# Kernel tuning notes

Measured on AMD Instinct MI355X. Metric: run time of the kernel, lower is better.

## Reference

```python
import jax, jax.numpy as jnp
import numpy as np

B, T, D, H = 64, 512, 768, 96


def setup_inputs() -> dict:
    key = jax.random.key(0)
    kx, kq, kk, kv = jax.random.split(key, 4)
    x = jax.random.normal(kx, (B, T, D), dtype=jnp.float32)
    # Linear weights stored as [in, out]; scaled like torch default init
    s = 1.0 / np.sqrt(D)
    Wq = jax.random.normal(kq, (D, H), dtype=jnp.float32) * s
    Wk = jax.random.normal(kk, (D, H), dtype=jnp.float32) * s
    Wv = jax.random.normal(kv, (D, H), dtype=jnp.float32) * s
    return {"x": x, "Wq": Wq, "Wk": Wk, "Wv": Wv}


def reference(x, Wq, Wk, Wv):
    # q,k,v: [B,T,H]
    q = jnp.einsum('btd,dh->bth', x, Wq)
    k = jnp.einsum('btd,dh->bth', x, Wk)
    v = jnp.einsum('btd,dh->bth', x, Wv)
    scale = 1.0 / jnp.sqrt(jnp.array(q.shape[-1], dtype=x.dtype))
    # scores: [B,T,T]
    wei = jnp.einsum('bqh,bkh->bqk', q, k) * scale
    causal = jnp.tril(jnp.ones((T, T), dtype=bool))
    wei = jnp.where(causal, wei, jnp.array(-jnp.inf, dtype=wei.dtype))
    attn = jax.nn.softmax(wei, axis=-1)
    return jnp.einsum('bqk,bkh->bqh', attn, v)
```

## Files before the change

kernel.cpp:

```cpp
#include <hip/hip_runtime.h>
#include <hip/hip_bf16.h>
#include <math.h>

#define B_ 64
#define T_ 512
#define D_ 768
#define H_ 96
#define M_ (B_*T_)

typedef __attribute__((ext_vector_type(8))) short short8;
typedef __attribute__((ext_vector_type(4))) float f32x4;

__device__ __forceinline__ short f2bf(float f) {
  unsigned u = __float_as_uint(f);
  unsigned r = (u + 0x7FFFu + ((u >> 16) & 1u)) >> 16;
  return (short)r;
}

__global__ __launch_bounds__(256) void wt_kernel(
    const float* __restrict__ Wq, const float* __restrict__ Wk,
    const float* __restrict__ Wv, short* __restrict__ wt)
{
  int id = blockIdx.x * 256 + threadIdx.x;
  if (id >= 3*H_*D_) return;
  int n = id % 288;
  int k = id / 288;
  int mi = n / 96, cc = n % 96;
  const float* Wm = (mi == 0) ? Wq : ((mi == 1) ? Wk : Wv);
  wt[(size_t)n * D_ + k] = f2bf(Wm[(size_t)k * H_ + cc]);
}

#define BMP 64
#define BKP 32
#define ASTR 36

__global__ __launch_bounds__(256) void qkv_mfma_kernel(
    const float* __restrict__ x, const short* __restrict__ wt,
    short* __restrict__ qb, short* __restrict__ kb, short* __restrict__ vtp)
{
  __shared__ short as[2][BMP][ASTR];
  __shared__ short bs[2][288][ASTR];

  const int t    = threadIdx.x;
  const int row0 = blockIdx.x * BMP;
  const int lane = t & 63;
  const int w    = t >> 6;
  const int wr   = w >> 1;
  const int wc   = w & 1;
  const int l15  = lane & 15;
  const int l4   = lane >> 4;

  auto stage = [&](int buf, int k0) {
    {
      int m = t >> 2, k8 = t & 3;
      const float* src = x + (size_t)(row0 + m) * D_ + k0 + k8 * 8;
      float4 f0 = *reinterpret_cast<const float4*>(src);
      float4 f1 = *reinterpret_cast<const float4*>(src + 4);
      short8 v;
      v[0] = f2bf(f0.x); v[1] = f2bf(f0.y); v[2] = f2bf(f0.z); v[3] = f2bf(f0.w);
      v[4] = f2bf(f1.x); v[5] = f2bf(f1.y); v[6] = f2bf(f1.z); v[7] = f2bf(f1.w);
      *reinterpret_cast<short8*>(&as[buf][m][k8 * 8]) = v;
    }
    #pragma unroll
    for (int i = 0; i < 4; ++i) {
      int id = t + i * 256;
      int n = id >> 2, k8 = id & 3;
      short8 v = *reinterpret_cast<const short8*>(wt + (size_t)n * D_ + k0 + k8 * 8);
      *reinterpret_cast<short8*>(&bs[buf][n][k8 * 8]) = v;
    }
    if (t < 128) {
      int id = t + 1024;
      int n = id >> 2, k8 = id & 3;
      short8 v = *reinterpret_cast<const short8*>(wt + (size_t)n * D_ + k0 + k8 * 8);
      *reinterpret_cast<short8*>(&bs[buf][n][k8 * 8]) = v;
    }
  };

  f32x4 acc[2][9];
  #pragma unroll
  for (int ri = 0; ri < 2; ++ri)
    #pragma unroll
    for (int ci = 0; ci < 9; ++ci) acc[ri][ci] = (f32x4){0.f, 0.f, 0.f, 0.f};

  stage(0, 0);
  __syncthreads();

  for (int ks = 0; ks < D_ / BKP; ++ks) {
    int buf = ks & 1;
    if (ks + 1 < D_ / BKP) stage(buf ^ 1, (ks + 1) * BKP);

    short8 a[2];
    #pragma unroll
    for (int ri = 0; ri < 2; ++ri) {
      int m = wr * 32 + ri * 16 + l15;
      a[ri] = *reinterpret_cast<const short8*>(&as[buf][m][l4 * 8]);
    }
    #pragma unroll
    for (int ci = 0; ci < 9; ++ci) {
      int n = wc * 144 + ci * 16 + l15;
      short8 bfrag = *reinterpret_cast<const short8*>(&bs[buf][n][l4 * 8]);
      #pragma unroll
      for (int ri = 0; ri < 2; ++ri)
        acc[ri][ci] = __builtin_amdgcn_mfma_f32_16x16x32_bf16(
            a[ri], bfrag, acc[ri][ci], 0, 0, 0);
    }
    __syncthreads();
  }

  #pragma unroll
  for (int ci = 0; ci < 9; ++ci) {
    int ncol = wc * 144 + ci * 16;
    int mi   = ncol / 96;
    int cc   = ncol % 96 + l15;
    #pragma unroll
    for (int ri = 0; ri < 2; ++ri) {
      int rbase = row0 + wr * 32 + ri * 16 + l4 * 4;
      if (mi == 2) {
        int bb = rbase / T_, tl = rbase % T_;
        short4 pk;
        pk.x = f2bf(acc[ri][ci][0]); pk.y = f2bf(acc[ri][ci][1]);
        pk.z = f2bf(acc[ri][ci][2]); pk.w = f2bf(acc[ri][ci][3]);
        *reinterpret_cast<short4*>(vtp + ((size_t)bb * H_ + cc) * T_ + tl) = pk;
      } else {
        short* Om = (mi == 0) ? qb : kb;
        #pragma unroll
        for (int reg = 0; reg < 4; ++reg)
          Om[(size_t)(rbase + reg) * H_ + cc] = f2bf(acc[ri][ci][reg]);
      }
    }
  }
}

#define QB 32
#define KVB 32
#define KSTR 104
#define VSTR 40
#define PSTR 40

__global__ __launch_bounds__(128) void attn_mfma_kernel(
    const short* __restrict__ qb, const short* __restrict__ kb,
    const short* __restrict__ vtp, float* __restrict__ out)
{
  __shared__ short ks[KVB][KSTR];
  __shared__ short vs[H_][VSTR];
  __shared__ short ps[2][16][PSTR];

  const int t    = threadIdx.x;
  const int lane = t & 63;
  const int w    = t >> 6;
  const int l15  = lane & 15;
  const int l4   = lane >> 4;
  const int qi   = 15 - blockIdx.x;
  const int b    = blockIdx.y;
  const int q0   = qi * QB;

  short8 qf[3];
  {
    const short* qbase = qb + ((size_t)(b * T_) + q0 + w * 16 + l15) * H_;
    #pragma unroll
    for (int f = 0; f < 3; ++f)
      qf[f] = *reinterpret_cast<const short8*>(qbase + f * 32 + l4 * 8);
  }

  f32x4 acc[6];
  #pragma unroll
  for (int c = 0; c < 6; ++c) acc[c] = (f32x4){0.f, 0.f, 0.f, 0.f};
  float m_r[4] = {-INFINITY, -INFINITY, -INFINITY, -INFINITY};
  float l_r[4] = {0.f, 0.f, 0.f, 0.f};
  const float scale = 0.10206207261596576f;

  const int jmax = q0 + QB;
  for (int j0 = 0; j0 < jmax; j0 += KVB) {
    __syncthreads();
    {
      int row = t >> 2, seg = t & 3;
      const short* src = kb + ((size_t)(b * T_) + j0 + row) * H_ + seg * 24;
      short* dst = &ks[row][seg * 24];
      *reinterpret_cast<short8*>(dst)      = *reinterpret_cast<const short8*>(src);
      *reinterpret_cast<short8*>(dst + 8)  = *reinterpret_cast<const short8*>(src + 8);
      *reinterpret_cast<short8*>(dst + 16) = *reinterpret_cast<const short8*>(src + 16);
    }
    {
      #pragma unroll
      for (int i = 0; i < 3; ++i) {
        int c = t + i * 128;
        int h = c >> 2, k8 = c & 3;
        *reinterpret_cast<short8*>(&vs[h][k8 * 8]) =
            *reinterpret_cast<const short8*>(vtp + ((size_t)b * H_ + h) * T_ + j0 + k8 * 8);
      }
    }
    __syncthreads();

    f32x4 sfr[2];
    sfr[0] = (f32x4){0.f,0.f,0.f,0.f};
    sfr[1] = (f32x4){0.f,0.f,0.f,0.f};
    #pragma unroll
    for (int ct = 0; ct < 2; ++ct)
      #pragma unroll
      for (int f = 0; f < 3; ++f) {
        short8 kf = *reinterpret_cast<const short8*>(&ks[ct * 16 + l15][f * 32 + l4 * 8]);
        sfr[ct] = __builtin_amdgcn_mfma_f32_16x16x32_bf16(qf[f], kf, sfr[ct], 0, 0, 0);
      }

    const int qrow = q0 + w * 16 + l4 * 4;
    float p0[4], p1[4], fsc[4];
    #pragma unroll
    for (int reg = 0; reg < 4; ++reg) {
      float s0 = sfr[0][reg] * scale;
      float s1 = sfr[1][reg] * scale;
      if (j0 + l15      > qrow + reg) s0 = -INFINITY;
      if (j0 + l15 + 16 > qrow + reg) s1 = -INFINITY;
      float tm = fmaxf(s0, s1);
      #pragma unroll
      for (int o = 1; o < 16; o <<= 1) tm = fmaxf(tm, __shfl_xor(tm, o));
      float Mnew = fmaxf(m_r[reg], tm);
      p0[reg] = __expf(s0 - Mnew);
      p1[reg] = __expf(s1 - Mnew);
      float psum = p0[reg] + p1[reg];
      #pragma unroll
      for (int o = 1; o < 16; o <<= 1) psum += __shfl_xor(psum, o);
      fsc[reg] = __expf(m_r[reg] - Mnew);
      m_r[reg] = Mnew;
      l_r[reg] = l_r[reg] * fsc[reg] + psum;
    }
    #pragma unroll
    for (int c = 0; c < 6; ++c)
      #pragma unroll
      for (int reg = 0; reg < 4; ++reg) acc[c][reg] *= fsc[reg];

    #pragma unroll
    for (int reg = 0; reg < 4; ++reg) {
      ps[w][l4 * 4 + reg][l15]      = f2bf(p0[reg]);
      ps[w][l4 * 4 + reg][l15 + 16] = f2bf(p1[reg]);
    }
    short8 pa = *reinterpret_cast<const short8*>(&ps[w][l15][l4 * 8]);

    #pragma unroll
    for (int c = 0; c < 6; ++c) {
      short8 vf = *reinterpret_cast<const short8*>(&vs[c * 16 + l15][l4 * 8]);
      acc[c] = __builtin_amdgcn_mfma_f32_16x16x32_bf16(pa, vf, acc[c], 0, 0, 0);
    }
  }

  float inv[4];
  #pragma unroll
  for (int reg = 0; reg < 4; ++reg) inv[reg] = 1.f / l_r[reg];
  #pragma unroll
  for (int c = 0; c < 6; ++c) {
    #pragma unroll
    for (int reg = 0; reg < 4; ++reg) {
      size_t row = (size_t)(b * T_) + q0 + w * 16 + l4 * 4 + reg;
      out[row * H_ + c * 16 + l15] = acc[c][reg] * inv[reg];
    }
  }
}

extern "C" void kernel_launch(void* const* d_in, const int* in_sizes, int n_in,
                              void* d_out, int out_size, void* d_ws, size_t ws_size,
                              hipStream_t stream) {
  const float* x  = (const float*)d_in[0];
  const float* Wq = (const float*)d_in[1];
  const float* Wk = (const float*)d_in[2];
  const float* Wv = (const float*)d_in[3];

  short* wt  = (short*)d_ws;
  short* qb  = (short*)((char*)d_ws + 524288);
  short* kb  = qb + (size_t)M_ * H_;
  short* vtp = kb + (size_t)M_ * H_;
  float* outp = (float*)d_out;

  hipLaunchKernelGGL(wt_kernel, dim3((3*H_*D_ + 255)/256), dim3(256), 0, stream,
                     Wq, Wk, Wv, wt);
  hipLaunchKernelGGL(qkv_mfma_kernel, dim3(M_/BMP), dim3(256), 0, stream,
                     x, wt, qb, kb, vtp);
  hipLaunchKernelGGL(attn_mfma_kernel, dim3(T_/QB, B_), dim3(128), 0, stream,
                     qb, kb, vtp, outp);
}
```

Baseline: 80.79 us.

## Preload x tile into registers and swizzle weight LDS in QKV GEMM

The QKV projection kernel now loads each wave's full 16x768 slice of x straight from global memory into registers as bf16 fragments before the K loop, so the shared-memory A tile and its per-step staging go away. Each wave now covers 16 rows and all 288 output columns, and the weight tile in LDS is XOR-swizzled to cut bank conflicts. The launch bounds now request 2 blocks per CU. The 24 short8 A fragments plus 18 accumulators raise register pressure considerably, and all x loads are issued up front instead of overlapping with compute.

```diff
diff --git a/kernel.cpp b/kernel.cpp
--- a/kernel.cpp
+++ b/kernel.cpp
@@ -30,103 +30,89 @@
   wt[(size_t)n * D_ + k] = f2bf(Wm[(size_t)k * H_ + cc]);
 }
 
-#define BMP 64
 #define BKP 32
 #define ASTR 36
 
-__global__ __launch_bounds__(256) void qkv_mfma_kernel(
+__global__ __launch_bounds__(256, 2) void qkv_mfma_kernel(
     const float* __restrict__ x, const short* __restrict__ wt,
     short* __restrict__ qb, short* __restrict__ kb, short* __restrict__ vtp)
 {
-  __shared__ short as[2][BMP][ASTR];
   __shared__ short bs[2][288][ASTR];
 
   const int t    = threadIdx.x;
-  const int row0 = blockIdx.x * BMP;
+  const int row0 = blockIdx.x * 64;
   const int lane = t & 63;
-  const int w    = t >> 6;
-  const int wr   = w >> 1;
-  const int wc   = w & 1;
+  const int wid  = t >> 6;
   const int l15  = lane & 15;
   const int l4   = lane >> 4;
-
-  auto stage = [&](int buf, int k0) {
-    {
-      int m = t >> 2, k8 = t & 3;
-      const float* src = x + (size_t)(row0 + m) * D_ + k0 + k8 * 8;
-      float4 f0 = *reinterpret_cast<const float4*>(src);
-      float4 f1 = *reinterpret_cast<const float4*>(src + 4);
-      short8 v;
-      v[0] = f2bf(f0.x); v[1] = f2bf(f0.y); v[2] = f2bf(f0.z); v[3] = f2bf(f0.w);
-      v[4] = f2bf(f1.x); v[5] = f2bf(f1.y); v[6] = f2bf(f1.z); v[7] = f2bf(f1.w);
-      *reinterpret_cast<short8*>(&as[buf][m][k8 * 8]) = v;
-    }
+  const int swz  = l4 ^ (l15 & 3);
+
+  auto stageW = [&](int buf, int k0) {
     #pragma unroll
     for (int i = 0; i < 4; ++i) {
       int id = t + i * 256;
       int n = id >> 2, k8 = id & 3;
       short8 v = *reinterpret_cast<const short8*>(wt + (size_t)n * D_ + k0 + k8 * 8);
-      *reinterpret_cast<short8*>(&bs[buf][n][k8 * 8]) = v;
+      *reinterpret_cast<short8*>(&bs[buf][n][(k8 ^ (n & 3)) * 8]) = v;
     }
     if (t < 128) {
       int id = t + 1024;
       int n = id >> 2, k8 = id & 3;
       short8 v = *reinterpret_cast<const short8*>(wt + (size_t)n * D_ + k0 + k8 * 8);
-      *reinterpret_cast<short8*>(&bs[buf][n][k8 * 8]) = v;
+      *reinterpret_cast<short8*>(&bs[buf][n][(k8 ^ (n & 3)) * 8]) = v;
     }
   };
 
-  f32x4 acc[2][9];
-  #pragma unroll
-  for (int ri = 0; ri < 2; ++ri)
-    #pragma unroll
-    for (int ci = 0; ci < 9; ++ci) acc[ri][ci] = (f32x4){0.f, 0.f, 0.f, 0.f};
-
-  stage(0, 0);
+  short8 af[24];
+  {
+    const float* xr = x + (size_t)(row0 + wid * 16 + l15) * D_ + l4 * 8;
+    #pragma unroll
+    for (int s = 0; s < 24; ++s) {
+      float4 f0 = *reinterpret_cast<const float4*>(xr + s * 32);
+      float4 f1 = *reinterpret_cast<const float4*>(xr + s * 32 + 4);
+      short8 v;
+      v[0] = f2bf(f0.x); v[1] = f2bf(f0.y); v[2] = f2bf(f0.z); v[3] = f2bf(f0.w);
+      v[4] = f2bf(f1.x); v[5] = f2bf(f1.y); v[6] = f2bf(f1.z); v[7] = f2bf(f1.w);
+      af[s] = v;
+    }
+  }
+
+  f32x4 acc[18];
+  #pragma unroll
+  for (int ci = 0; ci < 18; ++ci) acc[ci] = (f32x4){0.f, 0.f, 0.f, 0.f};
+
+  stageW(0, 0);
   __syncthreads();
 
-  for (int ks = 0; ks < D_ / BKP; ++ks) {
+  #pragma unroll
+  for (int ks = 0; ks < 24; ++ks) {
     int buf = ks & 1;
-    if (ks + 1 < D_ / BKP) stage(buf ^ 1, (ks + 1) * BKP);
-
-    short8 a[2];
-    #pragma unroll
-    for (int ri = 0; ri < 2; ++ri) {
-      int m = wr * 32 + ri * 16 + l15;
-      a[ri] = *reinterpret_cast<const short8*>(&as[buf][m][l4 * 8]);
-    }
-    #pragma unroll
-    for (int ci = 0; ci < 9; ++ci) {
-      int n = wc * 144 + ci * 16 + l15;
-      short8 bfrag = *reinterpret_cast<const short8*>(&bs[buf][n][l4 * 8]);
-      #pragma unroll
-      for (int ri = 0; ri < 2; ++ri)
-        acc[ri][ci] = __builtin_amdgcn_mfma_f32_16x16x32_bf16(
-            a[ri], bfrag, acc[ri][ci], 0, 0, 0);
+    if (ks + 1 < 24) stageW(buf ^ 1, (ks + 1) * BKP);
+    #pragma unroll
+    for (int ci = 0; ci < 18; ++ci) {
+      int n = ci * 16 + l15;
+      short8 bfrag = *reinterpret_cast<const short8*>(&bs[buf][n][swz * 8]);
+      acc[ci] = __builtin_amdgcn_mfma_f32_16x16x32_bf16(af[ks], bfrag, acc[ci], 0, 0, 0);
     }
     __syncthreads();
   }
 
   #pragma unroll
-  for (int ci = 0; ci < 9; ++ci) {
-    int ncol = wc * 144 + ci * 16;
-    int mi   = ncol / 96;
-    int cc   = ncol % 96 + l15;
-    #pragma unroll
-    for (int ri = 0; ri < 2; ++ri) {
-      int rbase = row0 + wr * 32 + ri * 16 + l4 * 4;
-      if (mi == 2) {
-        int bb = rbase / T_, tl = rbase % T_;
-        short4 pk;
-        pk.x = f2bf(acc[ri][ci][0]); pk.y = f2bf(acc[ri][ci][1]);
-        pk.z = f2bf(acc[ri][ci][2]); pk.w = f2bf(acc[ri][ci][3]);
-        *reinterpret_cast<short4*>(vtp + ((size_t)bb * H_ + cc) * T_ + tl) = pk;
-      } else {
-        short* Om = (mi == 0) ? qb : kb;
-        #pragma unroll
-        for (int reg = 0; reg < 4; ++reg)
-          Om[(size_t)(rbase + reg) * H_ + cc] = f2bf(acc[ri][ci][reg]);
-      }
+  for (int ci = 0; ci < 18; ++ci) {
+    int mi = ci / 6;
+    int cc = (ci % 6) * 16 + l15;
+    int rbase = row0 + wid * 16 + l4 * 4;
+    if (mi == 2) {
+      int bb = rbase / T_, tl = rbase % T_;
+      short4 pk;
+      pk.x = f2bf(acc[ci][0]); pk.y = f2bf(acc[ci][1]);
+      pk.z = f2bf(acc[ci][2]); pk.w = f2bf(acc[ci][3]);
+      *reinterpret_cast<short4*>(vtp + ((size_t)bb * H_ + cc) * T_ + tl) = pk;
+    } else {
+      short* Om = (mi == 0) ? qb : kb;
+      #pragma unroll
+      for (int reg = 0; reg < 4; ++reg)
+        Om[(size_t)(rbase + reg) * H_ + cc] = f2bf(acc[ci][reg]);
     }
   }
 }
@@ -271,7 +257,7 @@
 
   hipLaunchKernelGGL(wt_kernel, dim3((3*H_*D_ + 255)/256), dim3(256), 0, stream,
                      Wq, Wk, Wv, wt);
-  hipLaunchKernelGGL(qkv_mfma_kernel, dim3(M_/BMP), dim3(256), 0, stream,
+  hipLaunchKernelGGL(qkv_mfma_kernel, dim3(M_/64), dim3(256), 0, stream,
                      x, wt, qb, kb, vtp);
   hipLaunchKernelGGL(attn_mfma_kernel, dim3(T_/QB, B_), dim3(128), 0, stream,
                      qb, kb, vtp, outp);
```

Result: slower. 95.37 us (+18.0%).
